# Kernel tuning notes

Hardware: AMD Instinct MI355X
Metric: run time of the kernel (lower is better)

Reference implementation:

```python
import jax, jax.numpy as jnp
import numpy as np

B, D, E, H = 8192, 2048, 8, 128

def setup_inputs() -> dict:
    key = jax.random.key(0)
    ks = jax.random.split(key, 9)
    s_d = 1.0 / np.sqrt(D)
    s_h = 1.0 / np.sqrt(H)
    return {
        "x": jax.random.normal(ks[0], (B, D), dtype=jnp.float32),
        "gate_w": jax.random.normal(ks[1], (D, E), dtype=jnp.float32) * s_d,
        "gate_b": jnp.zeros((E,), dtype=jnp.float32),
        "W1": jax.random.normal(ks[2], (E, D, H), dtype=jnp.float32) * s_d,
        "b1": jnp.zeros((E, H), dtype=jnp.float32),
        "W2": jax.random.normal(ks[3], (E, H, H), dtype=jnp.float32) * s_h,
        "b2": jnp.zeros((E, H), dtype=jnp.float32),
        "W3": jax.random.normal(ks[4], (E, H, D), dtype=jnp.float32) * s_h,
        "b3": jnp.zeros((E, D), dtype=jnp.float32),
    }

def reference(x, gate_w, gate_b, W1, b1, W2, b2, W3, b3):
    # Adaptive gate: softmax over experts
    gates = jax.nn.softmax(x @ gate_w + gate_b, axis=1)          # [B, E]
    # All experts as one batched (grouped) GEMM over the expert axis.
    h1 = jax.nn.silu(jnp.einsum('bd,edh->ebh', x, W1) + b1[:, None, :])   # [E, B, H]
    h2 = jax.nn.silu(jnp.einsum('ebh,ehk->ebk', h1, W2) + b2[:, None, :]) # [E, B, H]
    y = jnp.einsum('ebh,ehd->ebd', h2, W3) + b3[:, None, :]               # [E, B, D]
    # Gate-weighted sum over experts (fused reduction, no [B,E,D] stack kept)
    out = jnp.einsum('be,ebd->bd', gates, y)                     # [B, D]
    return out
```

## Files before the change

kernel.cpp:

```cpp
#include <hip/hip_runtime.h>


typedef __attribute__((ext_vector_type(8))) short short8;
typedef __attribute__((ext_vector_type(4))) float f32x4;

#define B_SZ 8192
#define D_SZ 2048
#define E_SZ 8
#define H_SZ 128

#define VMCNT(n) asm volatile("s_waitcnt vmcnt(" #n ")" ::: "memory")
#define BAR()    __builtin_amdgcn_s_barrier()

__device__ __forceinline__ short f2bf(float f) {
  unsigned u = __builtin_bit_cast(unsigned, f);
  unsigned r = (u + 0x7fffu + ((u >> 16) & 1u)) >> 16;
  return (short)r;
}

__device__ __forceinline__ float bf2f(short s) {
  return __builtin_bit_cast(float, (unsigned)((unsigned short)s) << 16);
}

__device__ __forceinline__ float silu_f(float v) {
  return v / (1.f + __expf(-v));
}

__device__ __forceinline__ void gload_lds16(const void* g, void* l) {
  __builtin_amdgcn_global_load_lds(
      (const __attribute__((address_space(1))) void*)g,
      (__attribute__((address_space(3))) void*)l,
      16, 0, 0);
}

template<int NKT>
__device__ __forceinline__ void core256(const short* __restrict__ A0,
                                        const short* __restrict__ A1,
                                        const short* __restrict__ B0,
                                        const short* __restrict__ B1,
                                        short* lds, f32x4 acc[8][4])
{
  const int tid  = threadIdx.x;
  const int lane = tid & 63;
  const int wid  = tid >> 6;
  const int wm = wid >> 2, wn = wid & 3;
  const int lm = lane & 15, lk = lane >> 4;
  const int wlds = (tid & ~63) * 8;

  auto STAGE = [&](int n2) {
    const int tau = n2 >> 1, ks = n2 & 1, b = tau & 1;
    gload_lds16(A0 + (size_t)tau*8192 + ks*4096 + tid*8,
                lds + b*32768 + ks*4096 + wlds);
    gload_lds16(A1 + (size_t)tau*8192 + ks*4096 + tid*8,
                lds + b*32768 + 8192 + ks*4096 + wlds);
    gload_lds16(B0 + (size_t)tau*8192 + ks*4096 + tid*8,
                lds + b*32768 + 16384 + ks*4096 + wlds);
    gload_lds16(B1 + (size_t)tau*8192 + ks*4096 + tid*8,
                lds + b*32768 + 24576 + ks*4096 + wlds);
  };

  STAGE(0); STAGE(1);
  VMCNT(4); BAR();

  for (int n = 0; n < 2*NKT; ++n) {
    const int ks = n & 1, b = (n >> 1) & 1;
    if (n + 2 < 2*NKT) STAGE(n + 2);
    short8 av[8], bv[4];
    #pragma unroll
    for (int f = 0; f < 8; ++f)
      av[f] = *(const short8*)(lds + b*32768 + wm*8192 + (ks*4+lk)*1024 + (f*16 + lm)*8);
    #pragma unroll
    for (int f = 0; f < 4; ++f)
      bv[f] = *(const short8*)(lds + b*32768 + 16384 + (wn>>1)*8192 + (ks*4+lk)*1024
                               + ((wn&1)*64 + f*16 + lm)*8);
    __builtin_amdgcn_s_setprio(1);
    #pragma unroll
    for (int i = 0; i < 8; ++i)
      #pragma unroll
      for (int j = 0; j < 4; ++j)
        acc[i][j] = __builtin_amdgcn_mfma_f32_16x16x32_bf16(av[i], bv[j], acc[i][j], 0, 0, 0);
    __builtin_amdgcn_s_setprio(0);
    if (n + 2 < 2*NKT)      { VMCNT(4); BAR(); }
    else if (n + 1 < 2*NKT) { VMCNT(0); BAR(); }
  }
}

__global__ __launch_bounds__(256)
void k_convert(const float* __restrict__ x,  const float* __restrict__ W1,
               const float* __restrict__ W2, const float* __restrict__ W3,
               short* __restrict__ xf, short* __restrict__ w1f,
               short* __restrict__ w2f, short* __restrict__ w3f)
{
  const int gi = blockIdx.x * 256 + threadIdx.x;
  if (gi < 2097152) {
    const int t = gi >> 10, r = gi & 1023;
    const int bt = t >> 5, kt = t & 31;
    const int kg = r >> 7, p = r & 127;
    const float* src = x + (size_t)(bt*128 + p)*2048 + kt*64 + kg*8;
    const float4 v0 = *(const float4*)src;
    const float4 v1 = *(const float4*)(src + 4);
    short8 o;
    o[0]=f2bf(v0.x); o[1]=f2bf(v0.y); o[2]=f2bf(v0.z); o[3]=f2bf(v0.w);
    o[4]=f2bf(v1.x); o[5]=f2bf(v1.y); o[6]=f2bf(v1.z); o[7]=f2bf(v1.w);
    *(short8*)(xf + (size_t)gi*8) = o;
  } else if (gi < 2097152 + 262144) {
    const int g = gi - 2097152;
    const int t = g >> 10, r = g & 1023;
    const int e = t >> 5, kt = t & 31;
    const int kg = r >> 7, p = r & 127;
    const int k0 = kt*64 + kg*8;
    short8 o;
    #pragma unroll
    for (int j = 0; j < 8; ++j)
      o[j] = f2bf(W1[(size_t)e*262144 + (size_t)(k0 + j)*128 + p]);
    *(short8*)(w1f + (size_t)g*8) = o;
  } else if (gi < 2097152 + 262144 + 16384) {
    const int g = gi - (2097152 + 262144);
    const int t = g >> 10, r = g & 1023;
    const int e = t >> 1, kt = t & 1;
    const int kg = r >> 7, p = r & 127;
    const int k0 = kt*64 + kg*8;
    short8 o;
    #pragma unroll
    for (int j = 0; j < 8; ++j)
      o[j] = f2bf(W2[(size_t)e*16384 + (size_t)(k0 + j)*128 + p]);
    *(short8*)(w2f + (size_t)g*8) = o;
  } else if (gi < 2637824) {
    const int g = gi - 2375680;
    const int t = g >> 10, r = g & 1023;
    const int nt = t >> 4, kt = t & 15;
    const int kg = r >> 7, p = r & 127;
    const int k0 = kt*64 + kg*8;
    short8 o;
    #pragma unroll
    for (int j = 0; j < 8; ++j) {
      const int k = k0 + j;
      o[j] = f2bf(W3[(size_t)(k >> 7)*262144 + (size_t)(k & 127)*2048 + nt*128 + p]);
    }
    *(short8*)(w3f + (size_t)g*8) = o;
  }
}

__global__ __launch_bounds__(256)
void k_gate(const float* __restrict__ x, const float* __restrict__ gw,
            const float* __restrict__ gb, float* __restrict__ gates)
{
  const int wid = threadIdx.x >> 6, lane = threadIdx.x & 63;
  const int row = blockIdx.x * 4 + wid;
  const float* xr = x + (size_t)row * 2048;
  float acc[8] = {0.f,0.f,0.f,0.f,0.f,0.f,0.f,0.f};
  for (int it = 0; it < 32; ++it) {
    const int k = it*64 + lane;
    const float xv = xr[k];
    const float4 g0 = *(const float4*)(gw + (size_t)k*8);
    const float4 g1 = *(const float4*)(gw + (size_t)k*8 + 4);
    acc[0] += xv*g0.x; acc[1] += xv*g0.y; acc[2] += xv*g0.z; acc[3] += xv*g0.w;
    acc[4] += xv*g1.x; acc[5] += xv*g1.y; acc[6] += xv*g1.z; acc[7] += xv*g1.w;
  }
  #pragma unroll
  for (int e = 0; e < 8; ++e) {
    #pragma unroll
    for (int d = 1; d < 64; d <<= 1)
      acc[e] += __shfl_xor(acc[e], d, 64);
  }
  if (lane == 0) {
    float lg[8], mx = -1e30f;
    #pragma unroll
    for (int e = 0; e < 8; ++e) { lg[e] = acc[e] + gb[e]; mx = fmaxf(mx, lg[e]); }
    float s = 0.f;
    #pragma unroll
    for (int e = 0; e < 8; ++e) { lg[e] = __expf(lg[e] - mx); s += lg[e]; }
    const float inv = 1.f / s;
    #pragma unroll
    for (int e = 0; e < 8; ++e) gates[(size_t)row*8 + e] = lg[e] * inv;
  }
}

__global__ __launch_bounds__(512, 2)
void k_gemm1s(const short* __restrict__ xf, const short* __restrict__ w1f,
              short* __restrict__ p)
{
  __shared__ short lds[65536];
  const int b = blockIdx.x;
  const int xcd = b & 7, idx = b >> 3;
  const int BT = xcd*4 + (idx >> 3);
  const int rem = idx & 7;
  const int NT = rem >> 1, kh = rem & 1;

  f32x4 acc[8][4] = {};
  core256<16>(xf  + ((size_t)(BT*2)  *32 + kh*16)*8192,
              xf  + ((size_t)(BT*2+1)*32 + kh*16)*8192,
              w1f + ((size_t)(2*NT)  *32 + kh*16)*8192,
              w1f + ((size_t)(2*NT+1)*32 + kh*16)*8192,
              lds, acc);

  const int tid = threadIdx.x, lane = tid & 63, wid = tid >> 6;
  const int wm = wid >> 2, wn = wid & 3, lm = lane & 15, lr = lane >> 4;
  short* pd = p + (size_t)kh*8388608;
  #pragma unroll
  for (int fm = 0; fm < 8; ++fm)
  #pragma unroll
  for (int i = 0; i < 4; ++i) {
    const int m = BT*256 + wm*128 + fm*16 + lr*4 + i;
    #pragma unroll
    for (int fn = 0; fn < 4; ++fn) {
      const int n = NT*256 + wn*64 + fn*16 + lm;
      pd[(size_t)m*1024 + n] = f2bf(acc[fm][fn][i]);
    }
  }
}

__global__ __launch_bounds__(256, 2)
void k_gemm2m(const short* __restrict__ p, const short* __restrict__ w2f,
              const float* __restrict__ b1, const float* __restrict__ b2,
              const float* __restrict__ gates, short* __restrict__ h2gf)
{
  __shared__ short lds[32768];
  const int bt2 = blockIdx.x, e = blockIdx.y;
  const int tid = threadIdx.x;
  const int wlds = (tid & ~63) * 8;

  #pragma unroll
  for (int q = 0; q < 8; ++q)
    gload_lds16(w2f + (size_t)e*16384 + q*2048 + tid*8,
                lds + 16384 + q*2048 + wlds);

  #pragma unroll
  for (int u = 0; u < 8; ++u) {
    const int g = u*256 + tid;
    const int m = g >> 4, hg = g & 15;
    const size_t src = (size_t)(bt2*128 + m)*1024 + e*128 + hg*8;
    const short8 a = *(const short8*)(p + src);
    const short8 c = *(const short8*)(p + 8388608 + src);
    short8 o;
    #pragma unroll
    for (int j = 0; j < 8; ++j) {
      const float v = bf2f(a[j]) + bf2f(c[j]) + b1[e*128 + hg*8 + j];
      o[j] = f2bf(silu_f(v));
    }
    *(short8*)(lds + (hg>>3)*8192 + (hg&7)*1024 + m*8) = o;
  }
  VMCNT(0);
  __syncthreads();

  const int lane = tid & 63, wid = tid >> 6;
  const int wr = wid >> 1, wc = wid & 1, lm = lane & 15, lk = lane >> 4, lr = lane >> 4;
  f32x4 acc[4][4] = {};
  #pragma unroll
  for (int kt = 0; kt < 2; ++kt)
  #pragma unroll
  for (int ks = 0; ks < 2; ++ks) {
    short8 av[4], bv[4];
    #pragma unroll
    for (int f = 0; f < 4; ++f)
      av[f] = *(const short8*)(lds + kt*8192 + (ks*4+lk)*1024 + (wr*64 + f*16 + lm)*8);
    #pragma unroll
    for (int f = 0; f < 4; ++f)
      bv[f] = *(const short8*)(lds + 16384 + kt*8192 + (ks*4+lk)*1024 + (wc*64 + f*16 + lm)*8);
    #pragma unroll
    for (int i = 0; i < 4; ++i)
      #pragma unroll
      for (int j = 0; j < 4; ++j)
        acc[i][j] = __builtin_amdgcn_mfma_f32_16x16x32_bf16(av[i], bv[j], acc[i][j], 0, 0, 0);
  }
  __syncthreads();

  #pragma unroll
  for (int fm = 0; fm < 4; ++fm)
  #pragma unroll
  for (int i = 0; i < 4; ++i) {
    const int m = wr*64 + fm*16 + lr*4 + i;
    const float g = gates[(size_t)(bt2*128 + m)*8 + e];
    #pragma unroll
    for (int fn = 0; fn < 4; ++fn) {
      const int h = wc*64 + fn*16 + lm;
      const float v = silu_f(acc[fm][fn][i] + b2[e*128 + h]) * g;
      lds[(h>>6)*8192 + ((h>>3)&7)*1024 + m*8 + (h&7)] = f2bf(v);
    }
  }
  __syncthreads();

  #pragma unroll
  for (int q = 0; q < 8; ++q) {
    const int g = q*256 + tid;
    const int li = g*8;
    const int t2 = li >> 13, o = li & 8191;
    *(short8*)(h2gf + ((size_t)bt2*16 + e*2 + t2)*8192 + o) = *(const short8*)(lds + li);
  }
}

__global__ __launch_bounds__(512, 2)
void k_gemm3(const short* __restrict__ h2gf, const short* __restrict__ w3f,
             const float* __restrict__ b3, const float* __restrict__ gates,
             float* __restrict__ out)
{
  __shared__ short lds[65536];
  const int wg = blockIdx.x;
  const int xcd = wg & 7, idx = wg >> 3;
  const int bt = xcd*4 + (idx & 3);
  const int nt = idx >> 2;

  f32x4 acc[8][4] = {};
  core256<16>(h2gf + (size_t)(bt*2)  *16*8192,
              h2gf + (size_t)(bt*2+1)*16*8192,
              w3f  + (size_t)(2*nt)  *16*8192,
              w3f  + (size_t)(2*nt+1)*16*8192,
              lds, acc);

  const int tid = threadIdx.x, lane = tid & 63, wid = tid >> 6;
  const int wm = wid >> 2, wn = wid & 3, lm = lane & 15, lr = lane >> 4;
  float b3c[4][8];
  #pragma unroll
  for (int fn = 0; fn < 4; ++fn) {
    const int n = nt*256 + wn*64 + fn*16 + lm;
    #pragma unroll
    for (int e = 0; e < 8; ++e) b3c[fn][e] = b3[(size_t)e*D_SZ + n];
  }
  #pragma unroll
  for (int fm = 0; fm < 8; ++fm)
  #pragma unroll
  for (int i = 0; i < 4; ++i) {
    const int m = bt*256 + wm*128 + fm*16 + lr*4 + i;
    const float4 ga  = *(const float4*)(gates + (size_t)m*8);
    const float4 gbv = *(const float4*)(gates + (size_t)m*8 + 4);
    #pragma unroll
    for (int fn = 0; fn < 4; ++fn) {
      const int n = nt*256 + wn*64 + fn*16 + lm;
      const float bias = ga.x*b3c[fn][0] + ga.y*b3c[fn][1] + ga.z*b3c[fn][2] + ga.w*b3c[fn][3]
                       + gbv.x*b3c[fn][4] + gbv.y*b3c[fn][5] + gbv.z*b3c[fn][6] + gbv.w*b3c[fn][7];
      out[(size_t)m*D_SZ + n] = acc[fm][fn][i] + bias;
    }
  }
}

extern "C" void kernel_launch(void* const* d_in, const int* in_sizes, int n_in,
                              void* d_out, int out_size, void* d_ws, size_t ws_size,
                              hipStream_t stream)
{
  (void)in_sizes; (void)n_in; (void)out_size; (void)ws_size;
  const float* x  = (const float*)d_in[0];
  const float* gw = (const float*)d_in[1];
  const float* gb = (const float*)d_in[2];
  const float* W1 = (const float*)d_in[3];
  const float* b1 = (const float*)d_in[4];
  const float* W2 = (const float*)d_in[5];
  const float* b2 = (const float*)d_in[6];
  const float* W3 = (const float*)d_in[7];
  const float* b3 = (const float*)d_in[8];
  float* out = (float*)d_out;

  char* ws = (char*)d_ws;
  short* xf    = (short*)ws;  ws += (size_t)B_SZ*D_SZ*2;
  short* w1f   = (short*)ws;  ws += (size_t)E_SZ*D_SZ*H_SZ*2;
  short* w2f   = (short*)ws;  ws += (size_t)E_SZ*H_SZ*H_SZ*2;
  short* w3f   = (short*)ws;  ws += (size_t)E_SZ*H_SZ*D_SZ*2;
  float* gates = (float*)ws;  ws += (size_t)B_SZ*E_SZ*4;
  short* p     = (short*)ws;  ws += (size_t)2*B_SZ*1024*2;
  short* h2gf  = (short*)ws;  ws += (size_t)B_SZ*E_SZ*H_SZ*2;

  k_convert<<<dim3(10304), dim3(256), 0, stream>>>(x, W1, W2, W3, xf, w1f, w2f, w3f);
  k_gate   <<<dim3(2048),  dim3(256), 0, stream>>>(x, gw, gb, gates);
  k_gemm1s <<<dim3(256),   dim3(512), 0, stream>>>(xf, w1f, p);
  k_gemm2m <<<dim3(64, 8), dim3(256), 0, stream>>>(p, w2f, b1, b2, gates, h2gf);
  k_gemm3  <<<dim3(256),   dim3(512), 0, stream>>>(h2gf, w3f, b3, gates, out);
}
```

Before: 150.8 us.

## Deepen GEMM core pipeline to four LDS stages with split half-step MFMA phases

```diff
diff --git a/kernel.cpp b/kernel.cpp
--- a/kernel.cpp
+++ b/kernel.cpp
@@ -10,6 +10,8 @@
 #define H_SZ 128
 
 #define VMCNT(n) asm volatile("s_waitcnt vmcnt(" #n ")" ::: "memory")
+#define LGKM0()  asm volatile("s_waitcnt lgkmcnt(0)" ::: "memory")
+#define SB0()    __builtin_amdgcn_sched_barrier(0)
 #define BAR()    __builtin_amdgcn_s_barrier()
 
 __device__ __forceinline__ short f2bf(float f) {
@@ -34,55 +36,78 @@
 }
 
 template<int NKT>
-__device__ __forceinline__ void core256(const short* __restrict__ A0,
-                                        const short* __restrict__ A1,
-                                        const short* __restrict__ B0,
-                                        const short* __restrict__ B1,
-                                        short* lds, f32x4 acc[8][4])
+__device__ __forceinline__ void core256p(const short* __restrict__ A0,
+                                         const short* __restrict__ A1,
+                                         const short* __restrict__ B0,
+                                         const short* __restrict__ B1,
+                                         short* lds, f32x4 acc[8][4])
 {
   const int tid  = threadIdx.x;
   const int lane = tid & 63;
   const int wid  = tid >> 6;
   const int wm = wid >> 2, wn = wid & 3;
   const int lm = lane & 15, lk = lane >> 4;
-  const int wlds = (tid & ~63) * 8;
-
-  auto STAGE = [&](int n2) {
-    const int tau = n2 >> 1, ks = n2 & 1, b = tau & 1;
-    gload_lds16(A0 + (size_t)tau*8192 + ks*4096 + tid*8,
-                lds + b*32768 + ks*4096 + wlds);
-    gload_lds16(A1 + (size_t)tau*8192 + ks*4096 + tid*8,
-                lds + b*32768 + 8192 + ks*4096 + wlds);
-    gload_lds16(B0 + (size_t)tau*8192 + ks*4096 + tid*8,
-                lds + b*32768 + 16384 + ks*4096 + wlds);
-    gload_lds16(B1 + (size_t)tau*8192 + ks*4096 + tid*8,
-                lds + b*32768 + 24576 + ks*4096 + wlds);
-  };
-
-  STAGE(0); STAGE(1);
-  VMCNT(4); BAR();
-
-  for (int n = 0; n < 2*NKT; ++n) {
-    const int ks = n & 1, b = (n >> 1) & 1;
-    if (n + 2 < 2*NKT) STAGE(n + 2);
-    short8 av[8], bv[4];
-    #pragma unroll
-    for (int f = 0; f < 8; ++f)
-      av[f] = *(const short8*)(lds + b*32768 + wm*8192 + (ks*4+lk)*1024 + (f*16 + lm)*8);
-    #pragma unroll
-    for (int f = 0; f < 4; ++f)
-      bv[f] = *(const short8*)(lds + b*32768 + 16384 + (wn>>1)*8192 + (ks*4+lk)*1024
-                               + ((wn&1)*64 + f*16 + lm)*8);
+  const int wl = (tid & ~63) * 8;
+
+  short8 av[8], bv[4];
+
+  auto STAGE2 = [&](int eta, int half) {
+    const int tau = eta >> 1, ks = eta & 1, hb = eta & 3;
+    const size_t go = (size_t)tau*8192 + ks*4096 + tid*8;
+    short* lo = lds + hb*16384 + wl;
+    if (half == 0) {
+      gload_lds16(A0 + go, lo);
+      gload_lds16(A1 + go, lo + 4096);
+    } else {
+      gload_lds16(B0 + go, lo + 8192);
+      gload_lds16(B1 + go, lo + 12288);
+    }
+  };
+  auto RD_A = [&](int eta) {
+    const short* p = lds + (eta & 3)*16384 + wm*4096 + lk*1024 + lm*8;
+    #pragma unroll
+    for (int f = 0; f < 8; ++f) av[f] = *(const short8*)(p + f*128);
+  };
+  auto RD_B2 = [&](int eta, int nh) {
+    const short* p = lds + (eta & 3)*16384 + 8192 + (wn >> 1)*4096 + lk*1024
+                   + ((wn & 1)*64 + nh*32 + lm)*8;
+    bv[nh*2]     = *(const short8*)(p);
+    bv[nh*2 + 1] = *(const short8*)(p + 128);
+  };
+  auto MFMA2 = [&](int nh) {
     __builtin_amdgcn_s_setprio(1);
     #pragma unroll
-    for (int i = 0; i < 8; ++i)
-      #pragma unroll
-      for (int j = 0; j < 4; ++j)
-        acc[i][j] = __builtin_amdgcn_mfma_f32_16x16x32_bf16(av[i], bv[j], acc[i][j], 0, 0, 0);
+    for (int i = 0; i < 8; ++i) {
+      acc[i][nh*2]     = __builtin_amdgcn_mfma_f32_16x16x32_bf16(av[i], bv[nh*2],     acc[i][nh*2],     0, 0, 0);
+      acc[i][nh*2 + 1] = __builtin_amdgcn_mfma_f32_16x16x32_bf16(av[i], bv[nh*2 + 1], acc[i][nh*2 + 1], 0, 0, 0);
+    }
     __builtin_amdgcn_s_setprio(0);
-    if (n + 2 < 2*NKT)      { VMCNT(4); BAR(); }
-    else if (n + 1 < 2*NKT) { VMCNT(0); BAR(); }
-  }
+  };
+  auto HALF = [&](int eta, bool stg) {
+    RD_A(eta); RD_B2(eta, 0);
+    if (stg) STAGE2(eta + 3, 0);
+    BAR(); LGKM0(); SB0();
+    MFMA2(0);
+    SB0(); BAR();
+    RD_B2(eta, 1);
+    if (stg) STAGE2(eta + 3, 1);
+    BAR(); LGKM0(); SB0();
+    MFMA2(1);
+    SB0();
+  };
+
+  STAGE2(0, 0); STAGE2(0, 1);
+  STAGE2(1, 0); STAGE2(1, 1);
+  STAGE2(2, 0); STAGE2(2, 1);
+  VMCNT(8); BAR(); SB0();
+
+  for (int eta = 0; eta < 2*NKT - 3; ++eta) {
+    HALF(eta, true);
+    VMCNT(8); BAR(); SB0();
+  }
+  HALF(2*NKT - 3, false); VMCNT(4); BAR(); SB0();
+  HALF(2*NKT - 2, false); VMCNT(0); BAR(); SB0();
+  HALF(2*NKT - 1, false);
 }
 
 __global__ __launch_bounds__(256)
@@ -188,11 +213,11 @@
   const int NT = rem >> 1, kh = rem & 1;
 
   f32x4 acc[8][4] = {};
-  core256<16>(xf  + ((size_t)(BT*2)  *32 + kh*16)*8192,
-              xf  + ((size_t)(BT*2+1)*32 + kh*16)*8192,
-              w1f + ((size_t)(2*NT)  *32 + kh*16)*8192,
-              w1f + ((size_t)(2*NT+1)*32 + kh*16)*8192,
-              lds, acc);
+  core256p<16>(xf  + ((size_t)(BT*2)  *32 + kh*16)*8192,
+               xf  + ((size_t)(BT*2+1)*32 + kh*16)*8192,
+               w1f + ((size_t)(2*NT)  *32 + kh*16)*8192,
+               w1f + ((size_t)(2*NT+1)*32 + kh*16)*8192,
+               lds, acc);
 
   const int tid = threadIdx.x, lane = tid & 63, wid = tid >> 6;
   const int wm = wid >> 2, wn = wid & 3, lm = lane & 15, lr = lane >> 4;
@@ -301,11 +326,11 @@
   const int nt = idx >> 2;
 
   f32x4 acc[8][4] = {};
-  core256<16>(h2gf + (size_t)(bt*2)  *16*8192,
-              h2gf + (size_t)(bt*2+1)*16*8192,
-              w3f  + (size_t)(2*nt)  *16*8192,
-              w3f  + (size_t)(2*nt+1)*16*8192,
-              lds, acc);
+  core256p<16>(h2gf + (size_t)(bt*2)  *16*8192,
+               h2gf + (size_t)(bt*2+1)*16*8192,
+               w3f  + (size_t)(2*nt)  *16*8192,
+               w3f  + (size_t)(2*nt+1)*16*8192,
+               lds, acc);
 
   const int tid = threadIdx.x, lane = tid & 63, wid = tid >> 6;
   const int wm = wid >> 2, wn = wid & 3, lm = lane & 15, lr = lane >> 4;
```

Result: no change. 149.1 us (-1.1%).

## Shrink GEMM1/GEMM3 tiles to 128x128 with 4-wave blocks and simpler pipeline

Applied to the files above, without the earlier changes.

```diff
diff --git a/kernel.cpp b/kernel.cpp
--- a/kernel.cpp
+++ b/kernel.cpp
@@ -8,9 +8,6 @@
 #define D_SZ 2048
 #define E_SZ 8
 #define H_SZ 128
-
-#define VMCNT(n) asm volatile("s_waitcnt vmcnt(" #n ")" ::: "memory")
-#define BAR()    __builtin_amdgcn_s_barrier()
 
 __device__ __forceinline__ short f2bf(float f) {
   unsigned u = __builtin_bit_cast(unsigned, f);
@@ -33,55 +30,44 @@
       16, 0, 0);
 }
 
-template<int NKT>
-__device__ __forceinline__ void core256(const short* __restrict__ A0,
-                                        const short* __restrict__ A1,
-                                        const short* __restrict__ B0,
-                                        const short* __restrict__ B1,
-                                        short* lds, f32x4 acc[8][4])
+template<int NHT>
+__device__ __forceinline__ void core128(const short* __restrict__ A,
+                                        const short* __restrict__ B,
+                                        short* lds, f32x4 acc[4][4])
 {
   const int tid  = threadIdx.x;
   const int lane = tid & 63;
   const int wid  = tid >> 6;
-  const int wm = wid >> 2, wn = wid & 3;
+  const int wr = wid >> 1, wc = wid & 1;
   const int lm = lane & 15, lk = lane >> 4;
-  const int wlds = (tid & ~63) * 8;
-
-  auto STAGE = [&](int n2) {
-    const int tau = n2 >> 1, ks = n2 & 1, b = tau & 1;
-    gload_lds16(A0 + (size_t)tau*8192 + ks*4096 + tid*8,
-                lds + b*32768 + ks*4096 + wlds);
-    gload_lds16(A1 + (size_t)tau*8192 + ks*4096 + tid*8,
-                lds + b*32768 + 8192 + ks*4096 + wlds);
-    gload_lds16(B0 + (size_t)tau*8192 + ks*4096 + tid*8,
-                lds + b*32768 + 16384 + ks*4096 + wlds);
-    gload_lds16(B1 + (size_t)tau*8192 + ks*4096 + tid*8,
-                lds + b*32768 + 24576 + ks*4096 + wlds);
+  const int wl = (tid & ~63) * 8;
+
+  auto STAGE = [&](int eta) {
+    const size_t go = (size_t)(eta >> 1)*8192 + (size_t)(eta & 1)*4096;
+    short* l = lds + (eta & 1)*8192;
+    gload_lds16(A + go + tid*8,        l + wl);
+    gload_lds16(A + go + 2048 + tid*8, l + 2048 + wl);
+    gload_lds16(B + go + tid*8,        l + 4096 + wl);
+    gload_lds16(B + go + 2048 + tid*8, l + 6144 + wl);
   };
 
-  STAGE(0); STAGE(1);
-  VMCNT(4); BAR();
-
-  for (int n = 0; n < 2*NKT; ++n) {
-    const int ks = n & 1, b = (n >> 1) & 1;
-    if (n + 2 < 2*NKT) STAGE(n + 2);
-    short8 av[8], bv[4];
-    #pragma unroll
-    for (int f = 0; f < 8; ++f)
-      av[f] = *(const short8*)(lds + b*32768 + wm*8192 + (ks*4+lk)*1024 + (f*16 + lm)*8);
-    #pragma unroll
-    for (int f = 0; f < 4; ++f)
-      bv[f] = *(const short8*)(lds + b*32768 + 16384 + (wn>>1)*8192 + (ks*4+lk)*1024
-                               + ((wn&1)*64 + f*16 + lm)*8);
-    __builtin_amdgcn_s_setprio(1);
-    #pragma unroll
-    for (int i = 0; i < 8; ++i)
+  STAGE(0);
+  __syncthreads();
+  for (int eta = 0; eta < NHT; ++eta) {
+    if (eta + 1 < NHT) STAGE(eta + 1);
+    const short* la = lds + (eta & 1)*8192 + lk*1024 + (wr*64 + lm)*8;
+    const short* lb = lds + (eta & 1)*8192 + 4096 + lk*1024 + (wc*64 + lm)*8;
+    short8 av[4], bv[4];
+    #pragma unroll
+    for (int f = 0; f < 4; ++f) av[f] = *(const short8*)(la + f*128);
+    #pragma unroll
+    for (int f = 0; f < 4; ++f) bv[f] = *(const short8*)(lb + f*128);
+    #pragma unroll
+    for (int i = 0; i < 4; ++i)
       #pragma unroll
       for (int j = 0; j < 4; ++j)
         acc[i][j] = __builtin_amdgcn_mfma_f32_16x16x32_bf16(av[i], bv[j], acc[i][j], 0, 0, 0);
-    __builtin_amdgcn_s_setprio(0);
-    if (n + 2 < 2*NKT)      { VMCNT(4); BAR(); }
-    else if (n + 1 < 2*NKT) { VMCNT(0); BAR(); }
+    __syncthreads();
   }
 }
 
@@ -176,35 +162,33 @@
   }
 }
 
-__global__ __launch_bounds__(512, 2)
+__global__ __launch_bounds__(256, 4)
 void k_gemm1s(const short* __restrict__ xf, const short* __restrict__ w1f,
               short* __restrict__ p)
 {
-  __shared__ short lds[65536];
+  __shared__ short lds[16384];
   const int b = blockIdx.x;
   const int xcd = b & 7, idx = b >> 3;
-  const int BT = xcd*4 + (idx >> 3);
-  const int rem = idx & 7;
-  const int NT = rem >> 1, kh = rem & 1;
-
-  f32x4 acc[8][4] = {};
-  core256<16>(xf  + ((size_t)(BT*2)  *32 + kh*16)*8192,
-              xf  + ((size_t)(BT*2+1)*32 + kh*16)*8192,
-              w1f + ((size_t)(2*NT)  *32 + kh*16)*8192,
-              w1f + ((size_t)(2*NT+1)*32 + kh*16)*8192,
+  const int bt = xcd*8 + (idx & 7);
+  const int rest = idx >> 3;
+  const int nt = rest & 7, kh = rest >> 3;
+
+  f32x4 acc[4][4] = {};
+  core128<32>(xf  + ((size_t)bt*32 + kh*16)*8192,
+              w1f + ((size_t)nt*32 + kh*16)*8192,
               lds, acc);
 
   const int tid = threadIdx.x, lane = tid & 63, wid = tid >> 6;
-  const int wm = wid >> 2, wn = wid & 3, lm = lane & 15, lr = lane >> 4;
+  const int wr = wid >> 1, wc = wid & 1, lm = lane & 15, lr = lane >> 4;
   short* pd = p + (size_t)kh*8388608;
   #pragma unroll
-  for (int fm = 0; fm < 8; ++fm)
+  for (int fm = 0; fm < 4; ++fm)
   #pragma unroll
   for (int i = 0; i < 4; ++i) {
-    const int m = BT*256 + wm*128 + fm*16 + lr*4 + i;
+    const int m = bt*128 + wr*64 + fm*16 + lr*4 + i;
     #pragma unroll
     for (int fn = 0; fn < 4; ++fn) {
-      const int n = NT*256 + wn*64 + fn*16 + lm;
+      const int n = nt*128 + wc*64 + fn*16 + lm;
       pd[(size_t)m*1024 + n] = f2bf(acc[fm][fn][i]);
     }
   }
@@ -240,7 +224,7 @@
     }
     *(short8*)(lds + (hg>>3)*8192 + (hg&7)*1024 + m*8) = o;
   }
-  VMCNT(0);
+  asm volatile("s_waitcnt vmcnt(0)" ::: "memory");
   __syncthreads();
 
   const int lane = tid & 63, wid = tid >> 6;
@@ -289,43 +273,41 @@
   }
 }
 
-__global__ __launch_bounds__(512, 2)
+__global__ __launch_bounds__(256, 4)
 void k_gemm3(const short* __restrict__ h2gf, const short* __restrict__ w3f,
              const float* __restrict__ b3, const float* __restrict__ gates,
              float* __restrict__ out)
 {
-  __shared__ short lds[65536];
-  const int wg = blockIdx.x;
-  const int xcd = wg & 7, idx = wg >> 3;
-  const int bt = xcd*4 + (idx & 3);
-  const int nt = idx >> 2;
-
-  f32x4 acc[8][4] = {};
-  core256<16>(h2gf + (size_t)(bt*2)  *16*8192,
-              h2gf + (size_t)(bt*2+1)*16*8192,
-              w3f  + (size_t)(2*nt)  *16*8192,
-              w3f  + (size_t)(2*nt+1)*16*8192,
+  __shared__ short lds[16384];
+  const int b = blockIdx.x;
+  const int xcd = b & 7, idx = b >> 3;
+  const int bt = xcd*8 + (idx & 7);
+  const int nt = idx >> 3;
+
+  f32x4 acc[4][4] = {};
+  core128<32>(h2gf + (size_t)bt*16*8192,
+              w3f  + (size_t)nt*16*8192,
               lds, acc);
 
   const int tid = threadIdx.x, lane = tid & 63, wid = tid >> 6;
-  const int wm = wid >> 2, wn = wid & 3, lm = lane & 15, lr = lane >> 4;
+  const int wr = wid >> 1, wc = wid & 1, lm = lane & 15, lr = lane >> 4;
   float b3c[4][8];
   #pragma unroll
   for (int fn = 0; fn < 4; ++fn) {
-    const int n = nt*256 + wn*64 + fn*16 + lm;
+    const int n = nt*128 + wc*64 + fn*16 + lm;
     #pragma unroll
     for (int e = 0; e < 8; ++e) b3c[fn][e] = b3[(size_t)e*D_SZ + n];
   }
   #pragma unroll
-  for (int fm = 0; fm < 8; ++fm)
+  for (int fm = 0; fm < 4; ++fm)
   #pragma unroll
   for (int i = 0; i < 4; ++i) {
-    const int m = bt*256 + wm*128 + fm*16 + lr*4 + i;
+    const int m = bt*128 + wr*64 + fm*16 + lr*4 + i;
     const float4 ga  = *(const float4*)(gates + (size_t)m*8);
     const float4 gbv = *(const float4*)(gates + (size_t)m*8 + 4);
     #pragma unroll
     for (int fn = 0; fn < 4; ++fn) {
-      const int n = nt*256 + wn*64 + fn*16 + lm;
+      const int n = nt*128 + wc*64 + fn*16 + lm;
       const float bias = ga.x*b3c[fn][0] + ga.y*b3c[fn][1] + ga.z*b3c[fn][2] + ga.w*b3c[fn][3]
                        + gbv.x*b3c[fn][4] + gbv.y*b3c[fn][5] + gbv.z*b3c[fn][6] + gbv.w*b3c[fn][7];
       out[(size_t)m*D_SZ + n] = acc[fm][fn][i] + bias;
@@ -360,7 +342,7 @@
 
   k_convert<<<dim3(10304), dim3(256), 0, stream>>>(x, W1, W2, W3, xf, w1f, w2f, w3f);
   k_gate   <<<dim3(2048),  dim3(256), 0, stream>>>(x, gw, gb, gates);
-  k_gemm1s <<<dim3(256),   dim3(512), 0, stream>>>(xf, w1f, p);
+  k_gemm1s <<<dim3(1024),  dim3(256), 0, stream>>>(xf, w1f, p);
   k_gemm2m <<<dim3(64, 8), dim3(256), 0, stream>>>(p, w2f, b1, b2, gates, h2gf);
-  k_gemm3  <<<dim3(256),   dim3(512), 0, stream>>>(h2gf, w3f, b3, gates, out);
-}
+  k_gemm3  <<<dim3(1024),  dim3(256), 0, stream>>>(h2gf, w3f, b3, gates, out);
+}
```

Result: slower. 156.8 us (+4.0%).
